# Performance work log

Hardware: AMD Instinct MI355X
Metric: run time of the kernel (lower is better)

The kernel has to match this reference:

```python
import jax, jax.numpy as jnp
import numpy as np

GROUPS = 8


def setup_inputs() -> dict:
    key = jax.random.key(0)
    k1, k2, k3 = jax.random.split(key, 3)
    B, H, W, Cin, Cout, KH, KW = 32, 56, 56, 256, 256, 3, 3
    inputs = jax.random.normal(k1, (B, H, W, Cin), dtype=jnp.float32)
    # HWIO kernel for grouped conv: input channel dim = Cin // groups
    fan_in = KH * KW * (Cin // GROUPS)
    limit = np.sqrt(6.0 / (fan_in + Cout // GROUPS))  # glorot-ish scale
    kernel = jax.random.uniform(k2, (KH, KW, Cin // GROUPS, Cout), dtype=jnp.float32,
                                minval=-limit, maxval=limit)
    bias = jnp.zeros((Cout,), dtype=jnp.float32)
    return {"inputs": inputs, "kernel": kernel, "bias": bias}


def reference(inputs, kernel, bias):
    # Equivalent to per-group slice + Conv2D + concat: a single grouped conv.
    # inputs: [B,H,W,Cin] NHWC; kernel: [KH,KW,Cin//G,Cout] HWIO
    out = jax.lax.conv_general_dilated(
        inputs, kernel,
        window_strides=(1, 1),
        padding="SAME",
        lhs_dilation=(1, 1),
        rhs_dilation=(1, 1),
        dimension_numbers=("NHWC", "HWIO", "NHWC"),
        feature_group_count=GROUPS,
    )
    out = out + bias  # broadcast over [B,H,W,Cout]
    return out
```

## Files before the change

kernel.cpp:

```cpp
#include <hip/hip_runtime.h>


#define R_ 4
#define NCHUNK (6 * 58 * 8)

typedef __bf16 bf16x8 __attribute__((ext_vector_type(8)));
typedef float floatx4 __attribute__((ext_vector_type(4)));
typedef unsigned short ushortx4 __attribute__((ext_vector_type(4)));

__device__ __forceinline__ unsigned short f2bf(float f) {
    unsigned int u = __builtin_bit_cast(unsigned int, f);
    u += 0x7fffu + ((u >> 16) & 1u);
    return (unsigned short)(u >> 16);
}

__global__ __launch_bounds__(256)
void wprep(const float* __restrict__ wgt, unsigned short* __restrict__ wbf) {
    const int i = blockIdx.x * 256 + threadIdx.x;
    const int co256 = i & 255;
    const int tmp   = i >> 8;
    const int ci    = tmp & 31;
    const int kk    = tmp >> 5;
    const int g  = co256 >> 5;
    const int co = co256 & 31;
    wbf[((g * 9 + kk) * 32 + co) * 32 + ci] = f2bf(wgt[i]);
}

__global__ __launch_bounds__(256, 7)
void gconv_mfma(const float* __restrict__ in, const unsigned short* __restrict__ wbf,
                const float* __restrict__ bias, float* __restrict__ out) {
    const int rt = blockIdx.x;
    const int g  = blockIdx.y;
    const int b  = blockIdx.z;
    const int y0 = rt * R_;

    __shared__ unsigned short lds_in[6 * 58 * 32];

    const int tid = threadIdx.x;

#pragma unroll
    for (int i = 0; i < 11; ++i) {
        const int c = tid + (i << 8);
        if (c < NCHUNK) {
            const int row = c / 464;
            const int rem = c - row * 464;
            const int col = rem >> 3;
            const int q   = rem & 7;
            const int gy = y0 - 1 + row;
            const int gx = col - 1;
            float4 v = make_float4(0.f, 0.f, 0.f, 0.f);
            if ((unsigned)gy < 56u && (unsigned)gx < 56u) {
                v = *reinterpret_cast<const float4*>(
                    &in[((((b * 56 + gy) * 56 + gx)) << 8) + (g << 5) + (q << 2)]);
            }
            ushortx4 p;
            p.x = f2bf(v.x); p.y = f2bf(v.y); p.z = f2bf(v.z); p.w = f2bf(v.w);
            *reinterpret_cast<ushortx4*>(&lds_in[(row * 58 + col) * 32 + (q << 2)]) = p;
        }
    }

    __syncthreads();

    const int wv   = tid >> 6;
    const int lane = tid & 63;
    const int lc   = lane & 15;
    const int quad = lane >> 4;

    const int nt = (wv < 2) ? 4 : 3;
    const int t0 = (wv < 2) ? (wv * 4) : (8 + (wv - 2) * 3);

    int lane_base[4];
#pragma unroll
    for (int t = 0; t < 4; ++t) {
        const int tt = (t < nt) ? (t0 + t) : 0;
        const int p  = tt * 16 + lc;
        const int yl = p / 56;
        lane_base[t] = (yl * 58 + (p - yl * 56)) * 32 + (quad << 3);
    }

    const unsigned short* wq = &wbf[(g * 9 * 32) * 32 + (quad << 3)];

    floatx4 acc[4][2];
#pragma unroll
    for (int t = 0; t < 4; ++t) { acc[t][0] = (floatx4)(0.f); acc[t][1] = (floatx4)(0.f); }

    bf16x8 b0 = *reinterpret_cast<const bf16x8*>(&wq[(0 * 32 + lc) * 32]);
    bf16x8 b1 = *reinterpret_cast<const bf16x8*>(&wq[(0 * 32 + 16 + lc) * 32]);

#pragma unroll
    for (int kk = 0; kk < 9; ++kk) {
        const int koff = ((kk / 3) * 58 + (kk % 3)) * 32;
        bf16x8 nb0 = b0, nb1 = b1;
        if (kk < 8) {
            nb0 = *reinterpret_cast<const bf16x8*>(&wq[((kk + 1) * 32 + lc) * 32]);
            nb1 = *reinterpret_cast<const bf16x8*>(&wq[((kk + 1) * 32 + 16 + lc) * 32]);
        }
#pragma unroll
        for (int t = 0; t < 4; ++t) {
            if (t < nt) {
                const bf16x8 a = *reinterpret_cast<const bf16x8*>(
                    &lds_in[lane_base[t] + koff]);
                acc[t][0] = __builtin_amdgcn_mfma_f32_16x16x32_bf16(b0, a, acc[t][0], 0, 0, 0);
                acc[t][1] = __builtin_amdgcn_mfma_f32_16x16x32_bf16(b1, a, acc[t][1], 0, 0, 0);
            }
        }
        b0 = nb0; b1 = nb1;
    }

    const float4 bv0 = *reinterpret_cast<const float4*>(&bias[(g << 5) + (quad << 2)]);
    const float4 bv1 = *reinterpret_cast<const float4*>(&bias[(g << 5) + 16 + (quad << 2)]);
    const int obase = (((b * 56 + y0) * 56) << 8) + (g << 5) + (quad << 2);
#pragma unroll
    for (int t = 0; t < 4; ++t) {
        if (t < nt) {
            const int p = (t0 + t) * 16 + lc;
            const int y = p / 56;
            const int x = p - y * 56;
            float* o = &out[obase + ((y * 56 + x) << 8)];
            float4 s0, s1;
            s0.x = acc[t][0][0] + bv0.x; s0.y = acc[t][0][1] + bv0.y;
            s0.z = acc[t][0][2] + bv0.z; s0.w = acc[t][0][3] + bv0.w;
            s1.x = acc[t][1][0] + bv1.x; s1.y = acc[t][1][1] + bv1.y;
            s1.z = acc[t][1][2] + bv1.z; s1.w = acc[t][1][3] + bv1.w;
            *reinterpret_cast<float4*>(o)      = s0;
            *reinterpret_cast<float4*>(o + 16) = s1;
        }
    }
}

__global__ __launch_bounds__(256, 2)
void gconv_mfma_ldsw(const float* __restrict__ in, const float* __restrict__ wgt,
                     const float* __restrict__ bias, float* __restrict__ out) {
    const int rt = blockIdx.x, g = blockIdx.y, b = blockIdx.z;
    const int y0 = rt * 8;
    __shared__ unsigned short lds_in[10 * 58 * 32];
    __shared__ unsigned short lds_w[9 * 32 * 32];
    const int tid = threadIdx.x;
    for (int i = tid; i < 9 * 32 * 32; i += 256) {
        const int co = i & 31, ci = (i >> 5) & 31, kk = i >> 10;
        lds_w[(kk * 32 + co) * 32 + ci] = f2bf(wgt[(kk * 32 + ci) * 256 + g * 32 + co]);
    }
    for (int c = tid; c < 10 * 58 * 8; c += 256) {
        const int row = c / 464, rem = c - row * 464, col = rem >> 3, q = rem & 7;
        const int gy = y0 - 1 + row, gx = col - 1;
        float4 v = make_float4(0.f, 0.f, 0.f, 0.f);
        if ((unsigned)gy < 56u && (unsigned)gx < 56u)
            v = *reinterpret_cast<const float4*>(&in[(((b * 56 + gy) * 56 + gx) * 256) + g * 32 + q * 4]);
        ushortx4 p;
        p.x = f2bf(v.x); p.y = f2bf(v.y); p.z = f2bf(v.z); p.w = f2bf(v.w);
        *reinterpret_cast<ushortx4*>(&lds_in[(row * 58 + col) * 32 + q * 4]) = p;
    }
    __syncthreads();
    const int wv = tid >> 6, lane = tid & 63, lc = lane & 15, quad = lane >> 4;
    int lane_base[7];
#pragma unroll
    for (int t = 0; t < 7; ++t) {
        const int p = (wv * 7 + t) * 16 + lc;
        const int yl = p / 56, xl = p - yl * 56;
        lane_base[t] = (yl * 58 + xl) * 32 + quad * 8;
    }
    floatx4 acc[7][2];
#pragma unroll
    for (int t = 0; t < 7; ++t) { acc[t][0] = (floatx4)(0.f); acc[t][1] = (floatx4)(0.f); }
#pragma unroll
    for (int kk = 0; kk < 9; ++kk) {
        const int ky = kk / 3, kx = kk % 3;
        const int koff = (ky * 58 + kx) * 32;
        const bf16x8 bf0 = *reinterpret_cast<const bf16x8*>(&lds_w[(kk * 32 + lc) * 32 + quad * 8]);
        const bf16x8 bf1 = *reinterpret_cast<const bf16x8*>(&lds_w[(kk * 32 + 16 + lc) * 32 + quad * 8]);
#pragma unroll
        for (int t = 0; t < 7; ++t) {
            const bf16x8 a = *reinterpret_cast<const bf16x8*>(&lds_in[lane_base[t] + koff]);
            acc[t][0] = __builtin_amdgcn_mfma_f32_16x16x32_bf16(a, bf0, acc[t][0], 0, 0, 0);
            acc[t][1] = __builtin_amdgcn_mfma_f32_16x16x32_bf16(a, bf1, acc[t][1], 0, 0, 0);
        }
    }
    const float bv0 = bias[g * 32 + lc], bv1 = bias[g * 32 + 16 + lc];
#pragma unroll
    for (int t = 0; t < 7; ++t)
#pragma unroll
        for (int r = 0; r < 4; ++r) {
            const int p = (wv * 7 + t) * 16 + quad * 4 + r;
            const int y = p / 56, x = p - y * 56;
            float* o = &out[(((b * 56) + y0 + y) * 56 + x) * 256 + g * 32];
            o[lc] = acc[t][0][r] + bv0;
            o[16 + lc] = acc[t][1][r] + bv1;
        }
}

extern "C" void kernel_launch(void* const* d_in, const int* in_sizes, int n_in,
                              void* d_out, int out_size, void* d_ws, size_t ws_size,
                              hipStream_t stream) {
    const float* in   = (const float*)d_in[0];
    const float* wgt  = (const float*)d_in[1];
    const float* bias = (const float*)d_in[2];
    float* out        = (float*)d_out;

    if (ws_size >= (size_t)(8 * 9 * 32 * 32 * sizeof(unsigned short))) {
        unsigned short* wbf = (unsigned short*)d_ws;
        wprep<<<dim3(288, 1, 1), dim3(256, 1, 1), 0, stream>>>(wgt, wbf);
        gconv_mfma<<<dim3(14, 8, 32), dim3(256, 1, 1), 0, stream>>>(in, wbf, bias, out);
    } else {
        gconv_mfma_ldsw<<<dim3(7, 8, 32), dim3(256, 1, 1), 0, stream>>>(in, wgt, bias, out);
    }
}
```

Before: 204.0 us.

## Pre-convert input to bf16 and stream tiles into LDS via global_load_lds

Adds a separate pass that converts the whole fp32 input tensor to bf16 in workspace. The conv kernel then fills its LDS halo tile with direct global-to-LDS 16-byte loads, using a zero-pad buffer for out-of-bounds pixels. This removes the per-block fp32 load, convert and LDS store from the conv kernel and halves its input traffic, but adds an extra full read and write of the input plus a large workspace requirement. The old path is kept as a fallback for when the workspace is too small.

```diff
diff --git a/kernel.cpp b/kernel.cpp
--- a/kernel.cpp
+++ b/kernel.cpp
@@ -2,11 +2,15 @@
 
 
 #define R_ 4
-#define NCHUNK (6 * 58 * 8)
 
 typedef __bf16 bf16x8 __attribute__((ext_vector_type(8)));
 typedef float floatx4 __attribute__((ext_vector_type(4)));
 typedef unsigned short ushortx4 __attribute__((ext_vector_type(4)));
+typedef unsigned short ushortx8 __attribute__((ext_vector_type(8)));
+
+#define IMG_USHORTS 25690112u
+#define WGT_USHORTS 73728u
+#define ZPAD_USHORTS 64u
 
 __device__ __forceinline__ unsigned short f2bf(float f) {
     unsigned int u = __builtin_bit_cast(unsigned int, f);
@@ -15,8 +19,24 @@
 }
 
 __global__ __launch_bounds__(256)
+void iprep(const float* __restrict__ in, unsigned short* __restrict__ obf) {
+    const int n8 = 3211264;
+    const int stride = gridDim.x * 256;
+    for (int i = blockIdx.x * 256 + threadIdx.x; i < n8; i += stride) {
+        const float4 a = *reinterpret_cast<const float4*>(&in[i * 8]);
+        const float4 b = *reinterpret_cast<const float4*>(&in[i * 8 + 4]);
+        ushortx8 p;
+        p[0] = f2bf(a.x); p[1] = f2bf(a.y); p[2] = f2bf(a.z); p[3] = f2bf(a.w);
+        p[4] = f2bf(b.x); p[5] = f2bf(b.y); p[6] = f2bf(b.z); p[7] = f2bf(b.w);
+        *reinterpret_cast<ushortx8*>(&obf[i * 8]) = p;
+    }
+}
+
+__global__ __launch_bounds__(256)
 void wprep(const float* __restrict__ wgt, unsigned short* __restrict__ wbf) {
     const int i = blockIdx.x * 256 + threadIdx.x;
+    if (blockIdx.x == 0 && threadIdx.x < ZPAD_USHORTS)
+        wbf[WGT_USHORTS + threadIdx.x] = 0;
     const int co256 = i & 255;
     const int tmp   = i >> 8;
     const int ci    = tmp & 31;
@@ -27,42 +47,39 @@
 }
 
 __global__ __launch_bounds__(256, 7)
-void gconv_mfma(const float* __restrict__ in, const unsigned short* __restrict__ wbf,
+void gconv_bf16(const unsigned short* __restrict__ bfin,
+                const unsigned short* __restrict__ wbf,
                 const float* __restrict__ bias, float* __restrict__ out) {
     const int rt = blockIdx.x;
     const int g  = blockIdx.y;
     const int b  = blockIdx.z;
     const int y0 = rt * R_;
 
-    __shared__ unsigned short lds_in[6 * 58 * 32];
-
-    const int tid = threadIdx.x;
-
-#pragma unroll
-    for (int i = 0; i < 11; ++i) {
-        const int c = tid + (i << 8);
-        if (c < NCHUNK) {
-            const int row = c / 464;
-            const int rem = c - row * 464;
-            const int col = rem >> 3;
-            const int q   = rem & 7;
-            const int gy = y0 - 1 + row;
-            const int gx = col - 1;
-            float4 v = make_float4(0.f, 0.f, 0.f, 0.f);
-            if ((unsigned)gy < 56u && (unsigned)gx < 56u) {
-                v = *reinterpret_cast<const float4*>(
-                    &in[((((b * 56 + gy) * 56 + gx)) << 8) + (g << 5) + (q << 2)]);
-            }
-            ushortx4 p;
-            p.x = f2bf(v.x); p.y = f2bf(v.y); p.z = f2bf(v.z); p.w = f2bf(v.w);
-            *reinterpret_cast<ushortx4*>(&lds_in[(row * 58 + col) * 32 + (q << 2)]) = p;
-        }
-    }
-
-    __syncthreads();
-
+    __shared__ unsigned short lds_in[352 * 32];
+
+    const int tid  = threadIdx.x;
     const int wv   = tid >> 6;
     const int lane = tid & 63;
+    const unsigned short* zpad = wbf + WGT_USHORTS;
+
+    for (int i = wv; i < 22; i += 4) {
+        const int s   = (i << 4) + (lane >> 2);
+        const int row = s / 58;
+        const int col = s - row * 58;
+        const unsigned gy = (unsigned)(y0 - 1 + row);
+        const unsigned gx = (unsigned)(col - 1);
+        const bool ok = (s < 348) & (gy < 56u) & (gx < 56u);
+        const unsigned short* src = ok
+            ? &bfin[(((b * 56 + (int)gy) * 56 + (int)gx) << 8) + (g << 5) + ((lane & 3) << 3)]
+            : zpad;
+        __builtin_amdgcn_global_load_lds(
+            (const __attribute__((address_space(1))) void*)src,
+            (__attribute__((address_space(3))) void*)&lds_in[i << 9],
+            16, 0, 0);
+    }
+
+    __syncthreads();
+
     const int lc   = lane & 15;
     const int quad = lane >> 4;
 
@@ -128,6 +145,84 @@
     }
 }
 
+__global__ __launch_bounds__(256, 7)
+void gconv_f32s(const float* __restrict__ in, const unsigned short* __restrict__ wbf,
+                const float* __restrict__ bias, float* __restrict__ out) {
+    const int rt = blockIdx.x, g = blockIdx.y, b = blockIdx.z;
+    const int y0 = rt * R_;
+    __shared__ unsigned short lds_in[6 * 58 * 32];
+    const int tid = threadIdx.x;
+#pragma unroll
+    for (int i = 0; i < 11; ++i) {
+        const int c = tid + (i << 8);
+        if (c < 6 * 58 * 8) {
+            const int row = c / 464, rem = c - row * 464, col = rem >> 3, q = rem & 7;
+            const int gy = y0 - 1 + row, gx = col - 1;
+            float4 v = make_float4(0.f, 0.f, 0.f, 0.f);
+            if ((unsigned)gy < 56u && (unsigned)gx < 56u)
+                v = *reinterpret_cast<const float4*>(
+                    &in[((((b * 56 + gy) * 56 + gx)) << 8) + (g << 5) + (q << 2)]);
+            ushortx4 p;
+            p.x = f2bf(v.x); p.y = f2bf(v.y); p.z = f2bf(v.z); p.w = f2bf(v.w);
+            *reinterpret_cast<ushortx4*>(&lds_in[(row * 58 + col) * 32 + (q << 2)]) = p;
+        }
+    }
+    __syncthreads();
+    const int wv = tid >> 6, lane = tid & 63, lc = lane & 15, quad = lane >> 4;
+    const int nt = (wv < 2) ? 4 : 3;
+    const int t0 = (wv < 2) ? (wv * 4) : (8 + (wv - 2) * 3);
+    int lane_base[4];
+#pragma unroll
+    for (int t = 0; t < 4; ++t) {
+        const int tt = (t < nt) ? (t0 + t) : 0;
+        const int p = tt * 16 + lc;
+        const int yl = p / 56;
+        lane_base[t] = (yl * 58 + (p - yl * 56)) * 32 + (quad << 3);
+    }
+    const unsigned short* wq = &wbf[(g * 9 * 32) * 32 + (quad << 3)];
+    floatx4 acc[4][2];
+#pragma unroll
+    for (int t = 0; t < 4; ++t) { acc[t][0] = (floatx4)(0.f); acc[t][1] = (floatx4)(0.f); }
+    bf16x8 b0 = *reinterpret_cast<const bf16x8*>(&wq[(0 * 32 + lc) * 32]);
+    bf16x8 b1 = *reinterpret_cast<const bf16x8*>(&wq[(0 * 32 + 16 + lc) * 32]);
+#pragma unroll
+    for (int kk = 0; kk < 9; ++kk) {
+        const int koff = ((kk / 3) * 58 + (kk % 3)) * 32;
+        bf16x8 nb0 = b0, nb1 = b1;
+        if (kk < 8) {
+            nb0 = *reinterpret_cast<const bf16x8*>(&wq[((kk + 1) * 32 + lc) * 32]);
+            nb1 = *reinterpret_cast<const bf16x8*>(&wq[((kk + 1) * 32 + 16 + lc) * 32]);
+        }
+#pragma unroll
+        for (int t = 0; t < 4; ++t) {
+            if (t < nt) {
+                const bf16x8 a = *reinterpret_cast<const bf16x8*>(&lds_in[lane_base[t] + koff]);
+                acc[t][0] = __builtin_amdgcn_mfma_f32_16x16x32_bf16(b0, a, acc[t][0], 0, 0, 0);
+                acc[t][1] = __builtin_amdgcn_mfma_f32_16x16x32_bf16(b1, a, acc[t][1], 0, 0, 0);
+            }
+        }
+        b0 = nb0; b1 = nb1;
+    }
+    const float4 bv0 = *reinterpret_cast<const float4*>(&bias[(g << 5) + (quad << 2)]);
+    const float4 bv1 = *reinterpret_cast<const float4*>(&bias[(g << 5) + 16 + (quad << 2)]);
+    const int obase = (((b * 56 + y0) * 56) << 8) + (g << 5) + (quad << 2);
+#pragma unroll
+    for (int t = 0; t < 4; ++t) {
+        if (t < nt) {
+            const int p = (t0 + t) * 16 + lc;
+            const int y = p / 56, x = p - y * 56;
+            float* o = &out[obase + ((y * 56 + x) << 8)];
+            float4 s0, s1;
+            s0.x = acc[t][0][0] + bv0.x; s0.y = acc[t][0][1] + bv0.y;
+            s0.z = acc[t][0][2] + bv0.z; s0.w = acc[t][0][3] + bv0.w;
+            s1.x = acc[t][1][0] + bv1.x; s1.y = acc[t][1][1] + bv1.y;
+            s1.z = acc[t][1][2] + bv1.z; s1.w = acc[t][1][3] + bv1.w;
+            *reinterpret_cast<float4*>(o)      = s0;
+            *reinterpret_cast<float4*>(o + 16) = s1;
+        }
+    }
+}
+
 __global__ __launch_bounds__(256, 2)
 void gconv_mfma_ldsw(const float* __restrict__ in, const float* __restrict__ wgt,
                      const float* __restrict__ bias, float* __restrict__ out) {
@@ -196,10 +291,19 @@
     const float* bias = (const float*)d_in[2];
     float* out        = (float*)d_out;
 
-    if (ws_size >= (size_t)(8 * 9 * 32 * 32 * sizeof(unsigned short))) {
+    const size_t need_full = (size_t)(IMG_USHORTS + WGT_USHORTS + ZPAD_USHORTS) * 2;
+    const size_t need_wgt  = (size_t)WGT_USHORTS * 2;
+
+    if (d_ws != nullptr && ws_size >= need_full) {
+        unsigned short* bfin = (unsigned short*)d_ws;
+        unsigned short* wbf  = bfin + IMG_USHORTS;
+        iprep<<<dim3(2048, 1, 1), dim3(256, 1, 1), 0, stream>>>(in, bfin);
+        wprep<<<dim3(288, 1, 1), dim3(256, 1, 1), 0, stream>>>(wgt, wbf);
+        gconv_bf16<<<dim3(14, 8, 32), dim3(256, 1, 1), 0, stream>>>(bfin, wbf, bias, out);
+    } else if (d_ws != nullptr && ws_size >= need_wgt) {
         unsigned short* wbf = (unsigned short*)d_ws;
         wprep<<<dim3(288, 1, 1), dim3(256, 1, 1), 0, stream>>>(wgt, wbf);
-        gconv_mfma<<<dim3(14, 8, 32), dim3(256, 1, 1), 0, stream>>>(in, wbf, bias, out);
+        gconv_f32s<<<dim3(14, 8, 32), dim3(256, 1, 1), 0, stream>>>(in, wbf, bias, out);
     } else {
         gconv_mfma_ldsw<<<dim3(7, 8, 32), dim3(256, 1, 1), 0, stream>>>(in, wgt, bias, out);
     }
```

New measurement: 225.4 us. 1.11x slower.

## Load conv input fragments directly from global memory, dropping LDS staging

Applied to the files above, without the earlier changes.

The main kernel no longer stages a bf16 halo tile in shared memory. Each lane reads its fp32 input fragments straight from global memory for every tap, using a zero-padded workspace region to handle borders, and converts them to bf16 in registers before the MFMA. The grid is flattened and swizzled so neighbouring blocks spread across XCDs, and the occupancy hint drops from 7 to 4 blocks per CU. This removes the LDS fill and barrier, but each input element is now fetched up to nine times and the code relies on cache hits to keep that affordable.

```diff
diff --git a/kernel.cpp b/kernel.cpp
--- a/kernel.cpp
+++ b/kernel.cpp
@@ -1,12 +1,15 @@
 #include <hip/hip_runtime.h>
+#include <hip/hip_bf16.h>
 
 
 #define R_ 4
-#define NCHUNK (6 * 58 * 8)
 
 typedef __bf16 bf16x8 __attribute__((ext_vector_type(8)));
 typedef float floatx4 __attribute__((ext_vector_type(4)));
 typedef unsigned short ushortx4 __attribute__((ext_vector_type(4)));
+
+#define WGT_USHORTS 73728u
+#define ZPAD_USHORTS 64u
 
 __device__ __forceinline__ unsigned short f2bf(float f) {
     unsigned int u = __builtin_bit_cast(unsigned int, f);
@@ -14,9 +17,20 @@
     return (unsigned short)(u >> 16);
 }
 
+__device__ __forceinline__ bf16x8 cvt_frag(float4 lo, float4 hi) {
+    union { bf16x8 v; __hip_bfloat162 h[4]; } u;
+    u.h[0] = __float22bfloat162_rn(make_float2(lo.x, lo.y));
+    u.h[1] = __float22bfloat162_rn(make_float2(lo.z, lo.w));
+    u.h[2] = __float22bfloat162_rn(make_float2(hi.x, hi.y));
+    u.h[3] = __float22bfloat162_rn(make_float2(hi.z, hi.w));
+    return u.v;
+}
+
 __global__ __launch_bounds__(256)
 void wprep(const float* __restrict__ wgt, unsigned short* __restrict__ wbf) {
     const int i = blockIdx.x * 256 + threadIdx.x;
+    if (blockIdx.x == 0 && threadIdx.x < ZPAD_USHORTS)
+        wbf[WGT_USHORTS + threadIdx.x] = 0;
     const int co256 = i & 255;
     const int tmp   = i >> 8;
     const int ci    = tmp & 31;
@@ -26,41 +40,18 @@
     wbf[((g * 9 + kk) * 32 + co) * 32 + ci] = f2bf(wgt[i]);
 }
 
-__global__ __launch_bounds__(256, 7)
-void gconv_mfma(const float* __restrict__ in, const unsigned short* __restrict__ wbf,
+__global__ __launch_bounds__(256, 4)
+void gconv_f32d(const float* __restrict__ in, const unsigned short* __restrict__ wbf,
                 const float* __restrict__ bias, float* __restrict__ out) {
-    const int rt = blockIdx.x;
-    const int g  = blockIdx.y;
-    const int b  = blockIdx.z;
+    const int h = blockIdx.x;
+    const int L = (h & 7) * 448 + (h >> 3);
+    const int rt = L % 14;
+    const int r2 = L / 14;
+    const int g  = r2 & 7;
+    const int b  = r2 >> 3;
     const int y0 = rt * R_;
 
-    __shared__ unsigned short lds_in[6 * 58 * 32];
-
-    const int tid = threadIdx.x;
-
-#pragma unroll
-    for (int i = 0; i < 11; ++i) {
-        const int c = tid + (i << 8);
-        if (c < NCHUNK) {
-            const int row = c / 464;
-            const int rem = c - row * 464;
-            const int col = rem >> 3;
-            const int q   = rem & 7;
-            const int gy = y0 - 1 + row;
-            const int gx = col - 1;
-            float4 v = make_float4(0.f, 0.f, 0.f, 0.f);
-            if ((unsigned)gy < 56u && (unsigned)gx < 56u) {
-                v = *reinterpret_cast<const float4*>(
-                    &in[((((b * 56 + gy) * 56 + gx)) << 8) + (g << 5) + (q << 2)]);
-            }
-            ushortx4 p;
-            p.x = f2bf(v.x); p.y = f2bf(v.y); p.z = f2bf(v.z); p.w = f2bf(v.w);
-            *reinterpret_cast<ushortx4*>(&lds_in[(row * 58 + col) * 32 + (q << 2)]) = p;
-        }
-    }
-
-    __syncthreads();
-
+    const int tid  = threadIdx.x;
     const int wv   = tid >> 6;
     const int lane = tid & 63;
     const int lc   = lane & 15;
@@ -69,13 +60,20 @@
     const int nt = (wv < 2) ? 4 : 3;
     const int t0 = (wv < 2) ? (wv * 4) : (8 + (wv - 2) * 3);
 
-    int lane_base[4];
+    const float* zsrc = (const float*)(wbf + WGT_USHORTS);
+
+    const float* cptr[4];
+    bool rlo[4], rhi[4], clo[4], chi[4];
 #pragma unroll
     for (int t = 0; t < 4; ++t) {
         const int tt = (t < nt) ? (t0 + t) : 0;
         const int p  = tt * 16 + lc;
         const int yl = p / 56;
-        lane_base[t] = (yl * 58 + (p - yl * 56)) * 32 + (quad << 3);
+        const int xl = p - yl * 56;
+        const int yy = y0 + yl;
+        cptr[t] = &in[(((b * 56 + yy) * 56 + xl) << 8) + (g << 5) + (quad << 3)];
+        rlo[t] = (yy > 0);  rhi[t] = (yy < 55);
+        clo[t] = (xl > 0);  chi[t] = (xl < 55);
     }
 
     const unsigned short* wq = &wbf[(g * 9 * 32) * 32 + (quad << 3)];
@@ -84,27 +82,25 @@
 #pragma unroll
     for (int t = 0; t < 4; ++t) { acc[t][0] = (floatx4)(0.f); acc[t][1] = (floatx4)(0.f); }
 
-    bf16x8 b0 = *reinterpret_cast<const bf16x8*>(&wq[(0 * 32 + lc) * 32]);
-    bf16x8 b1 = *reinterpret_cast<const bf16x8*>(&wq[(0 * 32 + 16 + lc) * 32]);
-
-#pragma unroll
-    for (int kk = 0; kk < 9; ++kk) {
-        const int koff = ((kk / 3) * 58 + (kk % 3)) * 32;
-        bf16x8 nb0 = b0, nb1 = b1;
-        if (kk < 8) {
-            nb0 = *reinterpret_cast<const bf16x8*>(&wq[((kk + 1) * 32 + lc) * 32]);
-            nb1 = *reinterpret_cast<const bf16x8*>(&wq[((kk + 1) * 32 + 16 + lc) * 32]);
-        }
-#pragma unroll
-        for (int t = 0; t < 4; ++t) {
-            if (t < nt) {
-                const bf16x8 a = *reinterpret_cast<const bf16x8*>(
-                    &lds_in[lane_base[t] + koff]);
-                acc[t][0] = __builtin_amdgcn_mfma_f32_16x16x32_bf16(b0, a, acc[t][0], 0, 0, 0);
-                acc[t][1] = __builtin_amdgcn_mfma_f32_16x16x32_bf16(b1, a, acc[t][1], 0, 0, 0);
+#pragma unroll
+    for (int t = 0; t < 4; ++t) {
+        if (t < nt) {
+#pragma unroll
+            for (int kk = 0; kk < 9; ++kk) {
+                const int dy = kk / 3 - 1, dx = kk % 3 - 1;
+                const int koff = (dy * 56 + dx) << 8;
+                const bool oky = (dy == 0) ? true : (dy < 0 ? rlo[t] : rhi[t]);
+                const bool okx = (dx == 0) ? true : (dx < 0 ? clo[t] : chi[t]);
+                const float* s = (oky && okx) ? (cptr[t] + koff) : zsrc;
+                const float4 lo = *reinterpret_cast<const float4*>(s);
+                const float4 hi = *reinterpret_cast<const float4*>(s + 4);
+                const bf16x8 wb0 = *reinterpret_cast<const bf16x8*>(&wq[(kk * 32 + lc) * 32]);
+                const bf16x8 wb1 = *reinterpret_cast<const bf16x8*>(&wq[(kk * 32 + 16 + lc) * 32]);
+                const bf16x8 a = cvt_frag(lo, hi);
+                acc[t][0] = __builtin_amdgcn_mfma_f32_16x16x32_bf16(wb0, a, acc[t][0], 0, 0, 0);
+                acc[t][1] = __builtin_amdgcn_mfma_f32_16x16x32_bf16(wb1, a, acc[t][1], 0, 0, 0);
             }
         }
-        b0 = nb0; b1 = nb1;
     }
 
     const float4 bv0 = *reinterpret_cast<const float4*>(&bias[(g << 5) + (quad << 2)]);
@@ -196,10 +192,12 @@
     const float* bias = (const float*)d_in[2];
     float* out        = (float*)d_out;
 
-    if (ws_size >= (size_t)(8 * 9 * 32 * 32 * sizeof(unsigned short))) {
+    const size_t need_wgt = (size_t)(WGT_USHORTS + ZPAD_USHORTS) * 2;
+
+    if (d_ws != nullptr && ws_size >= need_wgt) {
         unsigned short* wbf = (unsigned short*)d_ws;
         wprep<<<dim3(288, 1, 1), dim3(256, 1, 1), 0, stream>>>(wgt, wbf);
-        gconv_mfma<<<dim3(14, 8, 32), dim3(256, 1, 1), 0, stream>>>(in, wbf, bias, out);
+        gconv_f32d<<<dim3(3584, 1, 1), dim3(256, 1, 1), 0, stream>>>(in, wbf, bias, out);
     } else {
         gconv_mfma_ldsw<<<dim3(7, 8, 32), dim3(256, 1, 1), 0, stream>>>(in, wgt, bias, out);
     }
```

Measured after the change: 271.3 us. +33.0%, slower.
